# Kernel tuning notes

Hardware: AMD Instinct MI355X
Metric: run time of the kernel (lower is better)

## Reference

```python
import jax, jax.numpy as jnp
import numpy as np

HIDDEN = 1024
N_HEADS = 16
HEAD_DIM = HIDDEN // N_HEADS


def setup_inputs() -> dict:
    key = jax.random.key(0)
    ks = jax.random.split(key, 8)
    bs, seq = 8, 1024
    hidden_states = jax.random.normal(ks[0], (bs, seq, HIDDEN), dtype=jnp.float32)
    attention_mask = jnp.zeros((bs, 1, 1, seq), dtype=jnp.float32)
    s = 1.0 / np.sqrt(HIDDEN)
    Wq = jax.random.normal(ks[1], (HIDDEN, HIDDEN), dtype=jnp.float32) * s
    bq = jnp.zeros((HIDDEN,), dtype=jnp.float32)
    Wk = jax.random.normal(ks[2], (HIDDEN, HIDDEN), dtype=jnp.float32) * s
    bk = jnp.zeros((HIDDEN,), dtype=jnp.float32)
    Wv = jax.random.normal(ks[3], (HIDDEN, HIDDEN), dtype=jnp.float32) * s
    bv = jnp.zeros((HIDDEN,), dtype=jnp.float32)
    return {"hidden_states": hidden_states, "attention_mask": attention_mask,
            "Wq": Wq, "bq": bq, "Wk": Wk, "bk": bk, "Wv": Wv, "bv": bv}


def _split_heads(x):
    # [b, s, H] -> [b, h, s, d]
    b, s, _ = x.shape
    return x.reshape(b, s, N_HEADS, HEAD_DIM).transpose(0, 2, 1, 3)


def reference(hidden_states, attention_mask, Wq, bq, Wk, bk, Wv, bv):
    q = _split_heads(hidden_states @ Wq.T + bq)
    k = _split_heads(hidden_states @ Wk.T + bk)
    v = _split_heads(hidden_states @ Wv.T + bv)
    scale = 1.0 / np.sqrt(HEAD_DIM).astype(np.float32)
    scores = jnp.einsum('bhqd,bhkd->bhqk', q, k) * scale + attention_mask
    probs = jax.nn.softmax(scores, axis=-1)  # dropout p=0.0 -> identity
    ctx = jnp.einsum('bhqk,bhkd->bhqd', probs, v)
    b, h, s, d = ctx.shape
    return ctx.transpose(0, 2, 1, 3).reshape(b, s, h * d)
```

## Files before the change

kernel.cpp:

```cpp
#include <hip/hip_runtime.h>
#include <stdint.h>
#include <stddef.h>

#define HIDDEN 1024
#define NHEADS 16
#define HDIM   64
#define BS     8
#define SEQ    1024
#define MTOT   (BS*SEQ)
#define QKV_T  ((size_t)MTOT*HIDDEN)

typedef short    bf16x8 __attribute__((ext_vector_type(8)));
typedef float    f32x4  __attribute__((ext_vector_type(4)));
typedef uint16_t u16x4  __attribute__((ext_vector_type(4)));

__device__ __forceinline__ uint16_t f2bf(float f) {
  union { float f; uint32_t u; } c; c.f = f;
  uint32_t u = c.u + 0x7FFFu + ((c.u >> 16) & 1u);
  return (uint16_t)(u >> 16);
}

__device__ __forceinline__ float exp2fast(float x) {
#if __has_builtin(__builtin_amdgcn_exp2f)
  return __builtin_amdgcn_exp2f(x);
#else
  return __expf(x * 0.69314718056f);
#endif
}

__device__ __forceinline__ void gload_lds16(const uint16_t* g, uint16_t* lds) {
  __builtin_amdgcn_global_load_lds(
      (const __attribute__((address_space(1))) uint32_t*)g,
      (__attribute__((address_space(3))) uint32_t*)lds, 16, 0, 0);
}

__global__ __launch_bounds__(256) void cvt_kernel(
    const float* __restrict__ hs, const float* __restrict__ wq,
    const float* __restrict__ wk, const float* __restrict__ wv,
    uint16_t* __restrict__ hsb, uint16_t* __restrict__ wcat)
{
  const int i4 = blockIdx.x * 256 + threadIdx.x;
  f32x4 v;
  u16x4 o;
  if (i4 < 2097152) {
    v = *((const f32x4*)hs + i4);
    o[0]=f2bf(v[0]); o[1]=f2bf(v[1]); o[2]=f2bf(v[2]); o[3]=f2bf(v[3]);
    *((u16x4*)hsb + i4) = o;
  } else {
    int j4 = i4 - 2097152;
    int w  = j4 >> 18;
    int r4 = j4 & 262143;
    const float* src = (w == 0) ? wq : ((w == 1) ? wk : wv);
    v = *((const f32x4*)src + r4);
    o[0]=f2bf(v[0]); o[1]=f2bf(v[1]); o[2]=f2bf(v[2]); o[3]=f2bf(v[3]);
    *((u16x4*)wcat + j4) = o;
  }
}

__global__ __launch_bounds__(256) void gemm_qkv(
    const uint16_t* __restrict__ hsb, const uint16_t* __restrict__ wcat,
    const float* __restrict__ bq, const float* __restrict__ bk,
    const float* __restrict__ bv, uint16_t* __restrict__ qbuf,
    uint16_t* __restrict__ kbuf, uint16_t* __restrict__ vtbuf)
{
  __shared__ uint16_t Alds[2][128*32];
  __shared__ uint16_t Blds[2][128*32];

  const int bid = blockIdx.x;
  const int wg  = (bid & 7) * 192 + (bid >> 3);
  const int tm  = wg / 24, tn = wg % 24;
  const int m0  = tm * 128, n0 = tn * 128;
  const int t   = threadIdx.x;
  const int l   = t & 63, w = t >> 6;
  const int wm  = w >> 1, wn = w & 1;

  f32x4 acc[4][4];
#pragma unroll
  for (int i = 0; i < 4; i++)
#pragma unroll
    for (int j = 0; j < 4; j++) acc[i][j] = (f32x4){0.f,0.f,0.f,0.f};

  const int r0   = (w * 2) * 16 + (l >> 2);
  const int r1   = (w * 2 + 1) * 16 + (l >> 2);
  const int g0s  = (l & 3) ^ ((r0 >> 1) & 3);
  const int g1s  = (l & 3) ^ ((r1 >> 1) & 3);
  const size_t aoff0 = (size_t)r0 * HIDDEN + g0s * 8;
  const size_t aoff1 = (size_t)r1 * HIDDEN + g1s * 8;

  auto STAGE = [&](int buf, int kt) {
    const uint16_t* Ab = hsb  + (size_t)m0 * HIDDEN + kt * 32;
    const uint16_t* Bb = wcat + (size_t)n0 * HIDDEN + kt * 32;
    gload_lds16(Ab + aoff0, &Alds[buf][(w * 2) * 512]);
    gload_lds16(Ab + aoff1, &Alds[buf][(w * 2 + 1) * 512]);
    gload_lds16(Bb + aoff0, &Blds[buf][(w * 2) * 512]);
    gload_lds16(Bb + aoff1, &Blds[buf][(w * 2 + 1) * 512]);
  };

  auto COMPUTE = [&](int buf) {
    bf16x8 af[4], bfr[4];
    const int G = l >> 4;
#pragma unroll
    for (int i = 0; i < 4; i++) {
      int ar = wm * 64 + i * 16 + (l & 15);
      int gs = (G ^ ((ar >> 1) & 3)) & 3;
      af[i] = *(const bf16x8*)&Alds[buf][ar * 32 + gs * 8];
    }
#pragma unroll
    for (int j = 0; j < 4; j++) {
      int br = wn * 64 + j * 16 + (l & 15);
      int gs = (G ^ ((br >> 1) & 3)) & 3;
      bfr[j] = *(const bf16x8*)&Blds[buf][br * 32 + gs * 8];
    }
#pragma unroll
    for (int i = 0; i < 4; i++)
#pragma unroll
      for (int j = 0; j < 4; j++)
        acc[i][j] = __builtin_amdgcn_mfma_f32_16x16x32_bf16(af[i], bfr[j], acc[i][j], 0, 0, 0);
  };

  STAGE(0, 0);
  __syncthreads();
#pragma unroll 1
  for (int kt = 0; kt < 32; ++kt) {
    int cur = kt & 1;
    if (kt < 31) STAGE(cur ^ 1, kt + 1);
    COMPUTE(cur);
    __syncthreads();
  }

#pragma unroll
  for (int j = 0; j < 4; j++) {
    int n     = n0 + wn * 64 + j * 16 + (l & 15);
    int which = n >> 10, nn = n & 1023;
    const float* bp = (which == 0) ? bq : ((which == 1) ? bk : bv);
    float bias = bp[nn];
    int hh = nn >> 6, dd = nn & 63;
#pragma unroll
    for (int i = 0; i < 4; i++) {
      if (which == 2) {
        int m_  = m0 + wm * 64 + i * 16 + (l >> 4) * 4;
        int b_  = m_ >> 10, s_ = m_ & 1023;
        size_t bhh = (size_t)(b_ * NHEADS + hh);
        uint64_t pk =  (uint64_t)f2bf(acc[i][j][0] + bias)
                    | ((uint64_t)f2bf(acc[i][j][1] + bias) << 16)
                    | ((uint64_t)f2bf(acc[i][j][2] + bias) << 32)
                    | ((uint64_t)f2bf(acc[i][j][3] + bias) << 48);
        *(uint64_t*)&vtbuf[(bhh * HDIM + dd) * SEQ + s_] = pk;
      } else {
#pragma unroll
        for (int r = 0; r < 4; r++) {
          int m  = m0 + wm * 64 + i * 16 + (l >> 4) * 4 + r;
          int b_ = m >> 10, s_ = m & 1023;
          float val = acc[i][j][r] + bias;
          size_t bhh = (size_t)(b_ * NHEADS + hh);
          if (which == 0)
            qbuf[(bhh * SEQ + s_) * HDIM + dd] = f2bf(val * 0.18033688011112042f);
          else
            kbuf[(bhh * SEQ + s_) * HDIM + dd] = f2bf(val);
        }
      }
    }
  }
}

__global__ __launch_bounds__(256) void attn_kernel(
    const uint16_t* __restrict__ qb, const uint16_t* __restrict__ kb,
    const uint16_t* __restrict__ vtb, const float* __restrict__ mask,
    float* __restrict__ out)
{
  __shared__ uint16_t Klds[64 * 64];
  __shared__ uint16_t Vlds[64 * 64];
  __shared__ uint16_t Plds[4][32 * 64];
  __shared__ float    mlds[SEQ];

  const int bid = blockIdx.x;
  const int wg  = (bid & 7) * 128 + (bid >> 3);
  const int bh  = wg >> 3;
  const int qt  = wg & 7;
  const int b   = bh >> 4, h = bh & 15;

  const uint16_t* Qg = qb  + (size_t)bh * SEQ * HDIM;
  const uint16_t* Kg = kb  + (size_t)bh * SEQ * HDIM;
  const uint16_t* Vg = vtb + (size_t)bh * HDIM * SEQ;

  const int t = threadIdx.x, l = t & 63, w = t >> 6;
  const int G = l >> 4, q16 = l & 15;

  for (int i = t; i < SEQ; i += 256)
    mlds[i] = mask[b * SEQ + i] * 1.44269504089f;

  const int q0w = qt * 128 + w * 32;
  bf16x8 qf[2][2];
#pragma unroll
  for (int qi = 0; qi < 2; ++qi)
#pragma unroll
    for (int k0 = 0; k0 < 2; ++k0)
      qf[qi][k0] = *(const bf16x8*)(Qg + (size_t)(q0w + qi * 16 + q16) * HDIM + k0 * 32 + G * 8);

  f32x4 O[4][2];
#pragma unroll
  for (int dt = 0; dt < 4; dt++) { O[dt][0] = (f32x4){0,0,0,0}; O[dt][1] = (f32x4){0,0,0,0}; }
  float mrow[2] = {-3e38f, -3e38f}, lrow[2] = {0.f, 0.f};

  __syncthreads();

  const int srow = t >> 2;
  const int sg0  = t & 3;
  uint16_t* Pw = &Plds[w][0];
  const int qsw = q16 & 7;

#pragma unroll 1
  for (int kt = 0; kt < 16; ++kt) {
#pragma unroll
    for (int ia = 0; ia < 2; ia++) {
      int g  = sg0 + ia * 4;
      int gs = (g ^ (srow & 7)) & 7;
      bf16x8 kv = *(const bf16x8*)(Kg + (size_t)(kt * 64 + srow) * HDIM + g * 8);
      bf16x8 vv = *(const bf16x8*)(Vg + (size_t)srow * SEQ + kt * 64 + g * 8);
      *(bf16x8*)&Klds[srow * 64 + gs * 8] = kv;
      *(bf16x8*)&Vlds[srow * 64 + gs * 8] = vv;
    }
    __syncthreads();

    f32x4 mv[4];
#pragma unroll
    for (int jn = 0; jn < 4; jn++)
      mv[jn] = *(const f32x4*)&mlds[kt * 64 + jn * 16 + G * 4];

#pragma unroll
    for (int qi = 0; qi < 2; ++qi) {
      f32x4 sc[4];
#pragma unroll
      for (int jn = 0; jn < 4; jn++) sc[jn] = (f32x4){0,0,0,0};
      __builtin_amdgcn_s_setprio(1);
#pragma unroll
      for (int k0 = 0; k0 < 2; ++k0)
#pragma unroll
        for (int jn = 0; jn < 4; jn++) {
          int kr = jn * 16 + q16;
          int gs = ((k0 * 4 + G) ^ qsw) & 7;
          bf16x8 kf = *(const bf16x8*)&Klds[kr * 64 + gs * 8];
          sc[jn] = __builtin_amdgcn_mfma_f32_16x16x32_bf16(kf, qf[qi][k0], sc[jn], 0, 0, 0);
        }
      __builtin_amdgcn_s_setprio(0);

      float pm = -3e38f;
#pragma unroll
      for (int jn = 0; jn < 4; jn++) {
        sc[jn] += mv[jn];
        pm = fmaxf(pm, fmaxf(fmaxf(sc[jn][0], sc[jn][1]), fmaxf(sc[jn][2], sc[jn][3])));
      }
      pm = fmaxf(pm, __shfl_xor(pm, 16));
      pm = fmaxf(pm, __shfl_xor(pm, 32));
      if (!__all(pm <= mrow[qi] + 11.0f)) {
        float mn = fmaxf(mrow[qi], pm);
        float fs = exp2fast(mrow[qi] - mn);
        mrow[qi] = mn;
        lrow[qi] *= fs;
#pragma unroll
        for (int dt = 0; dt < 4; dt++) O[dt][qi] *= fs;
      }
      float ps = 0.f;
      const int q = qi * 16 + q16;
#pragma unroll
      for (int jn = 0; jn < 4; jn++) {
        float p0 = exp2fast(sc[jn][0] - mrow[qi]);
        float p1 = exp2fast(sc[jn][1] - mrow[qi]);
        float p2 = exp2fast(sc[jn][2] - mrow[qi]);
        float p3 = exp2fast(sc[jn][3] - mrow[qi]);
        ps += (p0 + p1) + (p2 + p3);
        uint2 pw2;
        pw2.x = (uint32_t)f2bf(p0) | ((uint32_t)f2bf(p1) << 16);
        pw2.y = (uint32_t)f2bf(p2) | ((uint32_t)f2bf(p3) << 16);
        int g16 = (jn * 2 + (G >> 1)) ^ qsw;
        *(uint2*)&Pw[q * 64 + g16 * 8 + (G & 1) * 4] = pw2;
      }
      ps += __shfl_xor(ps, 16);
      ps += __shfl_xor(ps, 32);
      lrow[qi] += ps;
    }

    __builtin_amdgcn_s_setprio(1);
#pragma unroll
    for (int ks = 0; ks < 2; ++ks) {
      int gp  = ks * 4 + G;
      int gsp = (gp ^ qsw) & 7;
      bf16x8 pf0 = *(const bf16x8*)&Pw[(q16     ) * 64 + gsp * 8];
      bf16x8 pf1 = *(const bf16x8*)&Pw[(16 + q16) * 64 + gsp * 8];
#pragma unroll
      for (int dt = 0; dt < 4; dt++) {
        int dr = dt * 16 + q16;
        bf16x8 vf = *(const bf16x8*)&Vlds[dr * 64 + gsp * 8];
        O[dt][0] = __builtin_amdgcn_mfma_f32_16x16x32_bf16(vf, pf0, O[dt][0], 0, 0, 0);
        O[dt][1] = __builtin_amdgcn_mfma_f32_16x16x32_bf16(vf, pf1, O[dt][1], 0, 0, 0);
      }
    }
    __builtin_amdgcn_s_setprio(0);
    __syncthreads();
  }

#pragma unroll
  for (int qi = 0; qi < 2; ++qi) {
    float inv = 1.0f / lrow[qi];
    int q = q0w + qi * 16 + q16;
    float* orow = out + (size_t)(b * SEQ + q) * HIDDEN + h * HDIM;
#pragma unroll
    for (int dt = 0; dt < 4; dt++) {
      f32x4 o4 = O[dt][qi] * inv;
      *(f32x4*)(orow + dt * 16 + G * 4) = o4;
    }
  }
}

extern "C" void kernel_launch(void* const* d_in, const int* in_sizes, int n_in,
                              void* d_out, int out_size, void* d_ws, size_t ws_size,
                              hipStream_t stream) {
  const float* hs   = (const float*)d_in[0];
  const float* mask = (const float*)d_in[1];
  const float* Wq   = (const float*)d_in[2];
  const float* bq   = (const float*)d_in[3];
  const float* Wk   = (const float*)d_in[4];
  const float* bk   = (const float*)d_in[5];
  const float* Wv   = (const float*)d_in[6];
  const float* bv   = (const float*)d_in[7];
  float* out = (float*)d_out;

  uint16_t* hsb  = (uint16_t*)d_ws;
  uint16_t* wcat = (uint16_t*)((char*)d_ws + 16777216u);
  uint16_t* qbuf = (uint16_t*)((char*)d_ws + 23068672u);
  uint16_t* kbuf = (uint16_t*)((char*)d_ws + 39845888u);
  uint16_t* vtbf = (uint16_t*)((char*)d_ws + 56623104u);

  cvt_kernel<<<11264, 256, 0, stream>>>(hs, Wq, Wk, Wv, hsb, wcat);
  gemm_qkv<<<1536, 256, 0, stream>>>(hsb, wcat, bq, bk, bv, qbuf, kbuf, vtbf);
  attn_kernel<<<1024, 256, 0, stream>>>(qbuf, kbuf, vtbf, mask, out);
}
```

Baseline: 165.1 us.

## Use direct global-to-LDS loads for K/V tiles, hardware bf16 pack, drop setprio

The attention kernel now loads K and V tiles with global_load_lds, which writes straight into LDS without staging through registers. The XOR swizzle moves to the source address so the LDS layout stays the same. Software bf16 rounding is replaced with the v_cvt_pk_bf16_f32 instruction in both the V-transpose epilogue and the P packing, and the s_setprio hints around the MFMA blocks are removed. These target register pressure, VALU work and load latency, though the loads are still not double-buffered and the priority change may alter wave scheduling.

```diff
diff --git a/kernel.cpp b/kernel.cpp
--- a/kernel.cpp
+++ b/kernel.cpp
@@ -18,6 +18,12 @@
   union { float f; uint32_t u; } c; c.f = f;
   uint32_t u = c.u + 0x7FFFu + ((c.u >> 16) & 1u);
   return (uint16_t)(u >> 16);
+}
+
+__device__ __forceinline__ uint32_t cvt_pk_bf16(float lo, float hi) {
+  uint32_t r;
+  asm("v_cvt_pk_bf16_f32 %0, %1, %2" : "=v"(r) : "v"(lo), "v"(hi));
+  return r;
 }
 
 __device__ __forceinline__ float exp2fast(float x) {
@@ -141,11 +147,10 @@
         int m_  = m0 + wm * 64 + i * 16 + (l >> 4) * 4;
         int b_  = m_ >> 10, s_ = m_ & 1023;
         size_t bhh = (size_t)(b_ * NHEADS + hh);
-        uint64_t pk =  (uint64_t)f2bf(acc[i][j][0] + bias)
-                    | ((uint64_t)f2bf(acc[i][j][1] + bias) << 16)
-                    | ((uint64_t)f2bf(acc[i][j][2] + bias) << 32)
-                    | ((uint64_t)f2bf(acc[i][j][3] + bias) << 48);
-        *(uint64_t*)&vtbuf[(bhh * HDIM + dd) * SEQ + s_] = pk;
+        uint2 pk;
+        pk.x = cvt_pk_bf16(acc[i][j][0] + bias, acc[i][j][1] + bias);
+        pk.y = cvt_pk_bf16(acc[i][j][2] + bias, acc[i][j][3] + bias);
+        *(uint2*)&vtbuf[(bhh * HDIM + dd) * SEQ + s_] = pk;
       } else {
 #pragma unroll
         for (int r = 0; r < 4; r++) {
@@ -204,8 +209,8 @@
 
   __syncthreads();
 
-  const int srow = t >> 2;
-  const int sg0  = t & 3;
+  const int srow8 = l >> 3;
+  const int gsrc  = (l & 7) ^ srow8;
   uint16_t* Pw = &Plds[w][0];
   const int qsw = q16 & 7;
 
@@ -213,12 +218,10 @@
   for (int kt = 0; kt < 16; ++kt) {
 #pragma unroll
     for (int ia = 0; ia < 2; ia++) {
-      int g  = sg0 + ia * 4;
-      int gs = (g ^ (srow & 7)) & 7;
-      bf16x8 kv = *(const bf16x8*)(Kg + (size_t)(kt * 64 + srow) * HDIM + g * 8);
-      bf16x8 vv = *(const bf16x8*)(Vg + (size_t)srow * SEQ + kt * 64 + g * 8);
-      *(bf16x8*)&Klds[srow * 64 + gs * 8] = kv;
-      *(bf16x8*)&Vlds[srow * 64 + gs * 8] = vv;
+      const int rbase = ia * 32 + w * 8;
+      const int row   = rbase + srow8;
+      gload_lds16(Kg + (size_t)(kt * 64 + row) * HDIM + gsrc * 8, &Klds[rbase * 64]);
+      gload_lds16(Vg + (size_t)row * SEQ + kt * 64 + gsrc * 8,    &Vlds[rbase * 64]);
     }
     __syncthreads();
 
@@ -232,7 +235,6 @@
       f32x4 sc[4];
 #pragma unroll
       for (int jn = 0; jn < 4; jn++) sc[jn] = (f32x4){0,0,0,0};
-      __builtin_amdgcn_s_setprio(1);
 #pragma unroll
       for (int k0 = 0; k0 < 2; ++k0)
 #pragma unroll
@@ -242,7 +244,6 @@
           bf16x8 kf = *(const bf16x8*)&Klds[kr * 64 + gs * 8];
           sc[jn] = __builtin_amdgcn_mfma_f32_16x16x32_bf16(kf, qf[qi][k0], sc[jn], 0, 0, 0);
         }
-      __builtin_amdgcn_s_setprio(0);
 
       float pm = -3e38f;
 #pragma unroll
@@ -270,8 +271,8 @@
         float p3 = exp2fast(sc[jn][3] - mrow[qi]);
         ps += (p0 + p1) + (p2 + p3);
         uint2 pw2;
-        pw2.x = (uint32_t)f2bf(p0) | ((uint32_t)f2bf(p1) << 16);
-        pw2.y = (uint32_t)f2bf(p2) | ((uint32_t)f2bf(p3) << 16);
+        pw2.x = cvt_pk_bf16(p0, p1);
+        pw2.y = cvt_pk_bf16(p2, p3);
         int g16 = (jn * 2 + (G >> 1)) ^ qsw;
         *(uint2*)&Pw[q * 64 + g16 * 8 + (G & 1) * 4] = pw2;
       }
@@ -280,7 +281,6 @@
       lrow[qi] += ps;
     }
 
-    __builtin_amdgcn_s_setprio(1);
 #pragma unroll
     for (int ks = 0; ks < 2; ++ks) {
       int gp  = ks * 4 + G;
@@ -295,7 +295,6 @@
         O[dt][1] = __builtin_amdgcn_mfma_f32_16x16x32_bf16(vf, pf1, O[dt][1], 0, 0, 0);
       }
     }
-    __builtin_amdgcn_s_setprio(0);
     __syncthreads();
   }
 
```

New measurement: 148.7 us. 1.11x faster.
